# Performance work log

Measured on AMD Instinct MI355X. Metric: run time of the kernel, lower is better.

## Reference

```python
import jax, jax.numpy as jnp
import numpy as np

EMBED = 768
HEADS = 12
HEAD_DIM = EMBED // HEADS  # 64


def setup_inputs() -> dict:
    key = jax.random.key(0)
    ks = jax.random.split(key, 9)
    d = HEAD_DIM
    s = 1.0 / np.sqrt(d)
    return {
        "x": jax.random.normal(ks[0], (8, 1024, EMBED), dtype=jnp.float32),
        "ln_w": jnp.ones((EMBED,), dtype=jnp.float32),
        "ln_b": jnp.zeros((EMBED,), dtype=jnp.float32),
        "Wq": jax.random.uniform(ks[1], (d, d), jnp.float32, -s, s),
        "bq": jax.random.uniform(ks[2], (d,), jnp.float32, -s, s),
        "Wk": jax.random.uniform(ks[3], (d, d), jnp.float32, -s, s),
        "bk": jax.random.uniform(ks[4], (d,), jnp.float32, -s, s),
        "Wv": jax.random.uniform(ks[5], (d, d), jnp.float32, -s, s),
        "bv": jax.random.uniform(ks[6], (d,), jnp.float32, -s, s),
    }


def reference(x, ln_w, ln_b, Wq, bq, Wk, bk, Wv, bv):
    bs, n, e = x.shape
    # LayerNorm over last dim (eps matches torch default 1e-5)
    mu = jnp.mean(x, axis=-1, keepdims=True)
    var = jnp.mean(jnp.square(x - mu), axis=-1, keepdims=True)
    xn = (x - mu) / jnp.sqrt(var + 1e-5) * ln_w + ln_b
    # Raw view split (NOT transpose split): [bs, n, E] -> [bs, H, n, d]
    xh = xn.reshape(bs, HEADS, n, HEAD_DIM)
    # Linear layers (torch Linear: y = x @ W.T + b)
    q = jnp.einsum("bhnd,ed->bhne", xh, Wq) + bq
    k = jnp.einsum("bhnd,ed->bhne", xh, Wk) + bk
    v = jnp.einsum("bhnd,ed->bhne", xh, Wv) + bv
    # Unusual: softmax FIRST, then divide by sqrt(d)
    scores = jnp.einsum("bhqd,bhkd->bhqk", q, k)
    attn = jax.nn.softmax(scores, axis=-1) / jnp.sqrt(jnp.float32(HEAD_DIM))
    feature = jnp.einsum("bhqk,bhkd->bhqd", attn, v)
    return feature.reshape(bs, n, e)
```

## Files before the change

kernel.cpp:

```cpp
#include <hip/hip_runtime.h>

#define EMBED 768
#define HEADS 12
#define HD 64
#define SEQ 1024
#define BS 8
#define NROWS (BS * HEADS * SEQ)
#define XP 72
#define PLP 40

typedef _Float16 f16;
typedef f16 f16x4 __attribute__((ext_vector_type(4)));
typedef f16 f16x8 __attribute__((ext_vector_type(8)));
typedef float f32x4 __attribute__((ext_vector_type(4)));

__global__ __launch_bounds__(256) void k_lnstats(const float* __restrict__ x,
                                                 const float* __restrict__ Wq,
                                                 const float* __restrict__ Wk,
                                                 const float* __restrict__ Wv,
                                                 float* __restrict__ mu_out,
                                                 float* __restrict__ rs_out,
                                                 f16* __restrict__ wf) {
    const int w = threadIdx.x >> 6;
    const int lane = threadIdx.x & 63;
    const int row = blockIdx.x * 4 + w;
    const float4* xr = (const float4*)(x + (long)row * EMBED);
    float s = 0.f, sq = 0.f;
#pragma unroll
    for (int kk = 0; kk < 3; ++kk) {
        float4 v = xr[lane + kk * 64];
        s += v.x + v.y + v.z + v.w;
        sq += v.x * v.x + v.y * v.y + v.z * v.z + v.w * v.w;
    }
#pragma unroll
    for (int off = 32; off; off >>= 1) {
        s += __shfl_xor(s, off, 64);
        sq += __shfl_xor(sq, off, 64);
    }
    if (lane == 0) {
        float mu = s * (1.f / EMBED);
        float var = sq * (1.f / EMBED) - mu * mu;
        mu_out[row] = mu;
        rs_out[row] = rsqrtf(var + 1e-5f);
    }
    if (blockIdx.x < 3) {
        const float* W = (blockIdx.x == 0) ? Wq : (blockIdx.x == 1) ? Wk : Wv;
        f16* dst = wf + (long)blockIdx.x * 4096;
        const int t = threadIdx.x;
#pragma unroll
        for (int i = 0; i < 2; ++i) {
            const int o = t * 2 + i;
            const int nt = o >> 7, half = (o >> 6) & 1, lp = o & 63;
            const int qd = lp >> 4, l16 = lp & 15;
            const float* src = W + (nt * 16 + l16) * 64 + half * 32 + qd * 8;
            float4 v0 = *(const float4*)src, v1 = *(const float4*)(src + 4);
            f16x8 h = {(f16)v0.x, (f16)v0.y, (f16)v0.z, (f16)v0.w,
                       (f16)v1.x, (f16)v1.y, (f16)v1.z, (f16)v1.w};
            *(f16x8*)(dst + o * 8) = h;
        }
    }
}

__global__ __launch_bounds__(256) void k_qkv(
    const float* __restrict__ x, const float* __restrict__ lw, const float* __restrict__ lb,
    const f16* __restrict__ wf,
    const float* __restrict__ bq, const float* __restrict__ bk, const float* __restrict__ bv,
    const float* __restrict__ mu, const float* __restrict__ rs,
    f16* __restrict__ qo, f16* __restrict__ ko, f16* __restrict__ vo) {
    __shared__ __align__(16) f16 xh[2][64 * XP];
    __shared__ __align__(16) f16 kb[2][4096];
    __shared__ __align__(16) f16 vb[2][4096];
    const int t = threadIdx.x;
    const unsigned r0 = (unsigned)blockIdx.x * 128;
    const int bh = (int)(r0 >> 10);
    const int seq0 = (int)(r0 & 1023);
    const int tile0 = seq0 >> 5;

#pragma unroll
    for (int st = 0; st < 2; ++st) {
        const unsigned fb = (r0 + st * 64u) * 64u + (unsigned)t * 16u;
        const unsigned xrow = fb / EMBED;
        const unsigned c0 = fb % EMBED;
        const float m_ = mu[xrow], s_ = rs[xrow];
        const int lrow = (t * 16) >> 6, lcol = (t * 16) & 63;
        f16* dst = &xh[st][lrow * XP + lcol];
        const float4* xp = (const float4*)(x + fb);
        const float4* wp = (const float4*)(lw + c0);
        const float4* bp = (const float4*)(lb + c0);
#pragma unroll
        for (int j = 0; j < 4; ++j) {
            float4 xv = xp[j], wv = wp[j], bv2 = bp[j];
            f16x4 h = {(f16)((xv.x - m_) * s_ * wv.x + bv2.x), (f16)((xv.y - m_) * s_ * wv.y + bv2.y),
                       (f16)((xv.z - m_) * s_ * wv.z + bv2.z), (f16)((xv.w - m_) * s_ * wv.w + bv2.w)};
            *(f16x4*)(dst + j * 4) = h;
        }
    }

    const int lane = t & 63, w = t >> 6, l16 = lane & 15, quad = lane >> 4;
    f16x8 a[2][2];
#pragma unroll
    for (int st = 0; st < 2; ++st) {
        a[st][0] = *(const f16x8*)&xh[st][(w * 16 + l16) * XP + quad * 8];
        a[st][1] = *(const f16x8*)&xh[st][(w * 16 + l16) * XP + 32 + quad * 8];
    }
    const float* Bs[3] = {bq, bk, bv};

#pragma unroll
    for (int m = 0; m < 3; ++m) {
        const f16* wfm = wf + (long)m * 4096 + lane * 8;
        f32x4 acc[2][4];
#pragma unroll
        for (int nt = 0; nt < 4; ++nt) {
            f16x8 b0 = *(const f16x8*)(wfm + (nt * 2 + 0) * 512);
            f16x8 b1 = *(const f16x8*)(wfm + (nt * 2 + 1) * 512);
            const float bias = Bs[m][nt * 16 + l16];
#pragma unroll
            for (int st = 0; st < 2; ++st) {
                f32x4 a_ = {0.f, 0.f, 0.f, 0.f};
                a_ = __builtin_amdgcn_mfma_f32_16x16x32_f16(a[st][0], b0, a_, 0, 0, 0);
                a_ = __builtin_amdgcn_mfma_f32_16x16x32_f16(a[st][1], b1, a_, 0, 0, 0);
#pragma unroll
                for (int rg = 0; rg < 4; ++rg) a_[rg] += bias;
                acc[st][nt] = a_;
            }
        }
        if (m == 0) {
#pragma unroll
            for (int st = 0; st < 2; ++st)
#pragma unroll
                for (int nt = 0; nt < 4; ++nt)
#pragma unroll
                    for (int rg = 0; rg < 4; ++rg)
                        xh[st][(w * 16 + quad * 4 + rg) * XP + nt * 16 + l16] = (f16)acc[st][nt][rg];
        } else if (m == 1) {
#pragma unroll
            for (int st = 0; st < 2; ++st)
#pragma unroll
                for (int nt = 0; nt < 4; ++nt) {
                    const int base = (w >> 1) * 2048 + ((w & 1) * 2 + (nt >> 1)) * 512 +
                                     ((((nt & 1) << 1) | (l16 >> 3))) * 128 + (quad * 4) * 8 + (l16 & 7);
#pragma unroll
                    for (int rg = 0; rg < 4; ++rg)
                        kb[st][base + rg * 8] = (f16)acc[st][nt][rg];
                }
        } else {
#pragma unroll
            for (int st = 0; st < 2; ++st)
#pragma unroll
                for (int nt = 0; nt < 4; ++nt) {
                    const int base = (w >> 1) * 2048 + nt * 512 + quad * 128 + l16 * 8 + (w & 1);
#pragma unroll
                    for (int rg = 0; rg < 4; ++rg)
                        vb[st][base + rg * 2] = (f16)acc[st][nt][rg];
                }
        }
    }

    __syncthreads();

#pragma unroll
    for (int st = 0; st < 2; ++st)
#pragma unroll
        for (int c = t; c < 512; c += 256) {
            const int row = c >> 3, c8 = (c & 7) * 8;
            *(f16x8*)(qo + ((long)r0 + st * 64 + row) * 64 + c8) = *(const f16x8*)&xh[st][row * XP + c8];
        }
    {
        f16* kg = ko + ((long)bh << 16) + (long)tile0 * 2048;
        f16* vg = vo + ((long)bh << 16) + (long)tile0 * 2048;
        const f16* kfl = &kb[0][0];
        const f16* vfl = &vb[0][0];
#pragma unroll
        for (int i = 0; i < 4; ++i) {
            const int o = (t + i * 256) * 8;
            *(f16x8*)(kg + o) = *(const f16x8*)(kfl + o);
            *(f16x8*)(vg + o) = *(const f16x8*)(vfl + o);
        }
    }
}

__global__ __launch_bounds__(256) void k_attn(const f16* __restrict__ q,
                                              const f16* __restrict__ k,
                                              const f16* __restrict__ vt,
                                              float* __restrict__ out) {
    __shared__ __align__(16) f16 pl[4][32 * PLP];
    const int t = threadIdx.x;
    const int w = t >> 6, lane = t & 63, l16 = lane & 15, quad = lane >> 4;
    const int bh = blockIdx.x;
    const int q0 = blockIdx.y * 128 + w * 32;
    const long hb = (long)bh * SEQ;
    const f16* kp0 = k + ((long)bh << 16) + lane * 8;
    const f16* vp0 = vt + ((long)bh << 16) + lane * 8;

    f16x8 qf[2][2];
#pragma unroll
    for (int mt = 0; mt < 2; ++mt) {
        const f16* qp = q + (hb + q0 + mt * 16 + l16) * 64 + quad * 8;
        qf[mt][0] = *(const f16x8*)qp;
        qf[mt][1] = *(const f16x8*)(qp + 32);
    }
    f32x4 o[2][4];
    f32x4 ls[2];
#pragma unroll
    for (int mt = 0; mt < 2; ++mt) {
        ls[mt] = (f32x4){0.f, 0.f, 0.f, 0.f};
#pragma unroll
        for (int nt = 0; nt < 4; ++nt) o[mt][nt] = (f32x4){0.f, 0.f, 0.f, 0.f};
    }
    f16x8 one;
#pragma unroll
    for (int j = 0; j < 8; ++j) one[j] = (f16)1.0f;
    const f32x4 m14 = {-14.f, -14.f, -14.f, -14.f};

#define LOADK(kt, kf)                                  \
    {                                                  \
        const f16* kp = kp0 + (kt) * 2048;             \
        kf[0] = *(const f16x8*)kp;                     \
        kf[1] = *(const f16x8*)(kp + 512);             \
        kf[2] = *(const f16x8*)(kp + 1024);            \
        kf[3] = *(const f16x8*)(kp + 1536);            \
    }
#define LOADV(kt, vf)                                  \
    {                                                  \
        const f16* vp = vp0 + (kt) * 2048;             \
        vf[0] = *(const f16x8*)vp;                     \
        vf[1] = *(const f16x8*)(vp + 512);             \
        vf[2] = *(const f16x8*)(vp + 1024);            \
        vf[3] = *(const f16x8*)(vp + 1536);            \
    }

    f16x8 ka[4], va[4], kb[4], vb[4];
    LOADK(0, ka);
    LOADV(0, va);

    auto body = [&](const f16x8* kf, const f16x8* vf) {
        f32x4 s[2][2];
#pragma unroll
        for (int mt = 0; mt < 2; ++mt) {
            f32x4 a = m14;
            a = __builtin_amdgcn_mfma_f32_16x16x32_f16(qf[mt][0], kf[0], a, 0, 0, 0);
            a = __builtin_amdgcn_mfma_f32_16x16x32_f16(qf[mt][1], kf[1], a, 0, 0, 0);
            s[mt][0] = a;
            f32x4 b = m14;
            b = __builtin_amdgcn_mfma_f32_16x16x32_f16(qf[mt][0], kf[2], b, 0, 0, 0);
            b = __builtin_amdgcn_mfma_f32_16x16x32_f16(qf[mt][1], kf[3], b, 0, 0, 0);
            s[mt][1] = b;
        }
#pragma unroll
        for (int mt = 0; mt < 2; ++mt)
#pragma unroll
            for (int rg = 0; rg < 4; ++rg) {
                float e0 = __expf(s[mt][0][rg]);
                float e1 = __expf(s[mt][1][rg]);
                auto pk = __builtin_amdgcn_cvt_pkrtz(e0, e1);
                *(decltype(pk)*)&pl[w][(mt * 16 + quad * 4 + rg) * PLP + l16 * 2] = pk;
            }
        f16x8 pf0 = *(const f16x8*)&pl[w][l16 * PLP + quad * 8];
        f16x8 pf1 = *(const f16x8*)&pl[w][(16 + l16) * PLP + quad * 8];
        ls[0] = __builtin_amdgcn_mfma_f32_16x16x32_f16(pf0, one, ls[0], 0, 0, 0);
        ls[1] = __builtin_amdgcn_mfma_f32_16x16x32_f16(pf1, one, ls[1], 0, 0, 0);
#pragma unroll
        for (int nt = 0; nt < 4; ++nt) {
            o[0][nt] = __builtin_amdgcn_mfma_f32_16x16x32_f16(pf0, vf[nt], o[0][nt], 0, 0, 0);
            o[1][nt] = __builtin_amdgcn_mfma_f32_16x16x32_f16(pf1, vf[nt], o[1][nt], 0, 0, 0);
        }
    };

    for (int kt = 0; kt < SEQ / 32; kt += 2) {
        LOADK(kt + 1, kb);
        LOADV(kt + 1, vb);
        body(ka, va);
        const int kn = (kt + 2 < SEQ / 32) ? kt + 2 : SEQ / 32 - 1;
        LOADK(kn, ka);
        LOADV(kn, va);
        body(kb, vb);
    }
#undef LOADK
#undef LOADV

#pragma unroll
    for (int mt = 0; mt < 2; ++mt) {
        float inv[4];
#pragma unroll
        for (int rg = 0; rg < 4; ++rg) inv[rg] = 1.f / (ls[mt][rg] * 8.0f);
#pragma unroll
        for (int nt = 0; nt < 4; ++nt) {
            float* op = out + (hb + q0 + mt * 16 + quad * 4) * 64 + nt * 16 + l16;
#pragma unroll
            for (int rg = 0; rg < 4; ++rg) op[(long)rg * 64] = o[mt][nt][rg] * inv[rg];
        }
    }
}

extern "C" void kernel_launch(void* const* d_in, const int* in_sizes, int n_in,
                              void* d_out, int out_size, void* d_ws, size_t ws_size,
                              hipStream_t stream) {
    const float* x = (const float*)d_in[0];
    const float* lw = (const float*)d_in[1];
    const float* lb = (const float*)d_in[2];
    const float* Wq = (const float*)d_in[3];
    const float* bq = (const float*)d_in[4];
    const float* Wk = (const float*)d_in[5];
    const float* bk = (const float*)d_in[6];
    const float* Wv = (const float*)d_in[7];
    const float* bv = (const float*)d_in[8];
    float* out = (float*)d_out;

    char* ws = (char*)d_ws;
    float* mu = (float*)ws;
    float* rs = (float*)(ws + 32768);
    f16* wfr = (f16*)(ws + 65536);
    f16* qo = (f16*)(ws + 98304);
    f16* ko = qo + (long)NROWS * 64;
    f16* vo = ko + (long)NROWS * 64;

    k_lnstats<<<2048, 256, 0, stream>>>(x, Wq, Wk, Wv, mu, rs, wfr);
    k_qkv<<<NROWS / 128, 256, 0, stream>>>(x, lw, lb, wfr, bq, bk, bv, mu, rs, qo, ko, vo);
    k_attn<<<dim3(BS * HEADS, SEQ / 128), 256, 0, stream>>>(qo, ko, vo, out);
}
```

Before: 138.8 us.

## Fold log2e into Q projection and double query rows per attention wave

Q weights and bias are pre-scaled by log2(e), so the softmax exponent can use the raw v_exp_f32 (base-2) instruction with no extra multiply. The attention kernel now runs 2 waves per block, each covering 64 query rows instead of 32. Every K/V fragment loaded is therefore reused across twice as many MFMA tiles, cutting global K/V traffic per query. In exchange each wave holds more accumulators and registers, which may lower occupancy, and fp16 rounding of Q changes slightly.

```diff
diff --git a/kernel.cpp b/kernel.cpp
--- a/kernel.cpp
+++ b/kernel.cpp
@@ -8,6 +8,7 @@
 #define NROWS (BS * HEADS * SEQ)
 #define XP 72
 #define PLP 40
+#define LOG2E 1.4426950408889634f
 
 typedef _Float16 f16;
 typedef f16 f16x4 __attribute__((ext_vector_type(4)));
@@ -45,6 +46,7 @@
     }
     if (blockIdx.x < 3) {
         const float* W = (blockIdx.x == 0) ? Wq : (blockIdx.x == 1) ? Wk : Wv;
+        const float sc = (blockIdx.x == 0) ? LOG2E : 1.0f;
         f16* dst = wf + (long)blockIdx.x * 4096;
         const int t = threadIdx.x;
 #pragma unroll
@@ -54,8 +56,8 @@
             const int qd = lp >> 4, l16 = lp & 15;
             const float* src = W + (nt * 16 + l16) * 64 + half * 32 + qd * 8;
             float4 v0 = *(const float4*)src, v1 = *(const float4*)(src + 4);
-            f16x8 h = {(f16)v0.x, (f16)v0.y, (f16)v0.z, (f16)v0.w,
-                       (f16)v1.x, (f16)v1.y, (f16)v1.z, (f16)v1.w};
+            f16x8 h = {(f16)(v0.x * sc), (f16)(v0.y * sc), (f16)(v0.z * sc), (f16)(v0.w * sc),
+                       (f16)(v1.x * sc), (f16)(v1.y * sc), (f16)(v1.z * sc), (f16)(v1.w * sc)};
             *(f16x8*)(dst + o * 8) = h;
         }
     }
@@ -108,12 +110,13 @@
 #pragma unroll
     for (int m = 0; m < 3; ++m) {
         const f16* wfm = wf + (long)m * 4096 + lane * 8;
+        const float bsc = (m == 0) ? LOG2E : 1.0f;
         f32x4 acc[2][4];
 #pragma unroll
         for (int nt = 0; nt < 4; ++nt) {
             f16x8 b0 = *(const f16x8*)(wfm + (nt * 2 + 0) * 512);
             f16x8 b1 = *(const f16x8*)(wfm + (nt * 2 + 1) * 512);
-            const float bias = Bs[m][nt * 16 + l16];
+            const float bias = Bs[m][nt * 16 + l16] * bsc;
 #pragma unroll
             for (int st = 0; st < 2; ++st) {
                 f32x4 a_ = {0.f, 0.f, 0.f, 0.f};
@@ -179,30 +182,30 @@
     }
 }
 
-__global__ __launch_bounds__(256) void k_attn(const f16* __restrict__ q,
+__global__ __launch_bounds__(128) void k_attn(const f16* __restrict__ q,
                                               const f16* __restrict__ k,
                                               const f16* __restrict__ vt,
                                               float* __restrict__ out) {
-    __shared__ __align__(16) f16 pl[4][32 * PLP];
+    __shared__ __align__(16) f16 pl[2][64 * PLP];
     const int t = threadIdx.x;
     const int w = t >> 6, lane = t & 63, l16 = lane & 15, quad = lane >> 4;
     const int bh = blockIdx.x;
-    const int q0 = blockIdx.y * 128 + w * 32;
+    const int q0 = blockIdx.y * 128 + w * 64;
     const long hb = (long)bh * SEQ;
     const f16* kp0 = k + ((long)bh << 16) + lane * 8;
     const f16* vp0 = vt + ((long)bh << 16) + lane * 8;
 
-    f16x8 qf[2][2];
-#pragma unroll
-    for (int mt = 0; mt < 2; ++mt) {
+    f16x8 qf[4][2];
+#pragma unroll
+    for (int mt = 0; mt < 4; ++mt) {
         const f16* qp = q + (hb + q0 + mt * 16 + l16) * 64 + quad * 8;
         qf[mt][0] = *(const f16x8*)qp;
         qf[mt][1] = *(const f16x8*)(qp + 32);
     }
-    f32x4 o[2][4];
-    f32x4 ls[2];
-#pragma unroll
-    for (int mt = 0; mt < 2; ++mt) {
+    f32x4 o[4][4];
+    f32x4 ls[4];
+#pragma unroll
+    for (int mt = 0; mt < 4; ++mt) {
         ls[mt] = (f32x4){0.f, 0.f, 0.f, 0.f};
 #pragma unroll
         for (int nt = 0; nt < 4; ++nt) o[mt][nt] = (f32x4){0.f, 0.f, 0.f, 0.f};
@@ -210,7 +213,8 @@
     f16x8 one;
 #pragma unroll
     for (int j = 0; j < 8; ++j) one[j] = (f16)1.0f;
-    const f32x4 m14 = {-14.f, -14.f, -14.f, -14.f};
+    const float C0 = -14.f * LOG2E;
+    const f32x4 cinit = {C0, C0, C0, C0};
 
 #define LOADK(kt, kf)                                  \
     {                                                  \
@@ -234,35 +238,35 @@
     LOADV(0, va);
 
     auto body = [&](const f16x8* kf, const f16x8* vf) {
-        f32x4 s[2][2];
-#pragma unroll
-        for (int mt = 0; mt < 2; ++mt) {
-            f32x4 a = m14;
+        f32x4 s[4][2];
+#pragma unroll
+        for (int mt = 0; mt < 4; ++mt) {
+            f32x4 a = cinit;
             a = __builtin_amdgcn_mfma_f32_16x16x32_f16(qf[mt][0], kf[0], a, 0, 0, 0);
             a = __builtin_amdgcn_mfma_f32_16x16x32_f16(qf[mt][1], kf[1], a, 0, 0, 0);
             s[mt][0] = a;
-            f32x4 b = m14;
+            f32x4 b = cinit;
             b = __builtin_amdgcn_mfma_f32_16x16x32_f16(qf[mt][0], kf[2], b, 0, 0, 0);
             b = __builtin_amdgcn_mfma_f32_16x16x32_f16(qf[mt][1], kf[3], b, 0, 0, 0);
             s[mt][1] = b;
         }
 #pragma unroll
-        for (int mt = 0; mt < 2; ++mt)
+        for (int mt = 0; mt < 4; ++mt)
 #pragma unroll
             for (int rg = 0; rg < 4; ++rg) {
-                float e0 = __expf(s[mt][0][rg]);
-                float e1 = __expf(s[mt][1][rg]);
+                float e0, e1;
+                asm("v_exp_f32 %0, %1" : "=v"(e0) : "v"(s[mt][0][rg]));
+                asm("v_exp_f32 %0, %1" : "=v"(e1) : "v"(s[mt][1][rg]));
                 auto pk = __builtin_amdgcn_cvt_pkrtz(e0, e1);
                 *(decltype(pk)*)&pl[w][(mt * 16 + quad * 4 + rg) * PLP + l16 * 2] = pk;
             }
-        f16x8 pf0 = *(const f16x8*)&pl[w][l16 * PLP + quad * 8];
-        f16x8 pf1 = *(const f16x8*)&pl[w][(16 + l16) * PLP + quad * 8];
-        ls[0] = __builtin_amdgcn_mfma_f32_16x16x32_f16(pf0, one, ls[0], 0, 0, 0);
-        ls[1] = __builtin_amdgcn_mfma_f32_16x16x32_f16(pf1, one, ls[1], 0, 0, 0);
-#pragma unroll
-        for (int nt = 0; nt < 4; ++nt) {
-            o[0][nt] = __builtin_amdgcn_mfma_f32_16x16x32_f16(pf0, vf[nt], o[0][nt], 0, 0, 0);
-            o[1][nt] = __builtin_amdgcn_mfma_f32_16x16x32_f16(pf1, vf[nt], o[1][nt], 0, 0, 0);
+#pragma unroll
+        for (int mt = 0; mt < 4; ++mt) {
+            f16x8 pf = *(const f16x8*)&pl[w][(mt * 16 + l16) * PLP + quad * 8];
+            ls[mt] = __builtin_amdgcn_mfma_f32_16x16x32_f16(pf, one, ls[mt], 0, 0, 0);
+#pragma unroll
+            for (int nt = 0; nt < 4; ++nt)
+                o[mt][nt] = __builtin_amdgcn_mfma_f32_16x16x32_f16(pf, vf[nt], o[mt][nt], 0, 0, 0);
         }
     };
 
@@ -279,7 +283,7 @@
 #undef LOADV
 
 #pragma unroll
-    for (int mt = 0; mt < 2; ++mt) {
+    for (int mt = 0; mt < 4; ++mt) {
         float inv[4];
 #pragma unroll
         for (int rg = 0; rg < 4; ++rg) inv[rg] = 1.f / (ls[mt][rg] * 8.0f);
@@ -316,5 +320,5 @@
 
     k_lnstats<<<2048, 256, 0, stream>>>(x, Wq, Wk, Wv, mu, rs, wfr);
     k_qkv<<<NROWS / 128, 256, 0, stream>>>(x, lw, lb, wfr, bq, bk, bv, mu, rs, qo, ko, vo);
-    k_attn<<<dim3(BS * HEADS, SEQ / 128), 256, 0, stream>>>(qo, ko, vo, out);
+    k_attn<<<dim3(BS * HEADS, SEQ / 128), 128, 0, stream>>>(qo, ko, vo, out);
 }
```

New measurement: 174.7 us. 1.26x slower.
